# Performance work log

Measured on AMD Instinct MI355X. Metric: run time of the kernel, lower is better.

The kernel has to match this reference:

```python
import jax, jax.numpy as jnp
import numpy as np

# SAN Subtraction hyperparameters (from init_kwargs)
K = 7        # kernel_size
STRIDE = 1
PAD = 3
DIL = 1
PAD_MODE = 1  # 0 -> zero pad, 1 -> reflect pad


def setup_inputs() -> dict:
    key = jax.random.key(0)
    x = jax.random.normal(key, (4, 64, 112, 112), dtype=jnp.float32)
    return {"x": x}


def reference(x):
    """out[n,c,kk,p] = x_center[n,c,p] - neighbor_kk[n,c,p]  (SAN Subtraction).

    Returns (N, C, K*K, H_out*W_out).
    """
    N, C, H, W = x.shape
    H_out = (H + 2 * PAD - DIL * (K - 1) - 1) // STRIDE + 1
    W_out = (W + 2 * PAD - DIL * (K - 1) - 1) // STRIDE + 1

    mode = "reflect" if PAD_MODE == 1 else "constant"
    xp = jnp.pad(x, ((0, 0), (0, 0), (PAD, PAD), (PAD, PAD)), mode=mode)

    off = jnp.arange(K) * DIL                      # (K,)
    r = jnp.arange(H_out)[:, None] * STRIDE + off  # (H_out, K)
    c = jnp.arange(W_out)[:, None] * STRIDE + off  # (W_out, K)

    # gather neighbors: broadcast index -> (N, C, H_out, K, W_out, K)
    nb = xp[:, :, r[:, :, None, None], c[None, None, :, :]]
    # -> (N, C, K_row, K_col, H_out, W_out) -> (N, C, K*K, H_out*W_out)
    nb = nb.transpose(0, 1, 3, 5, 2, 4).reshape(N, C, K * K, H_out * W_out)

    # center: unfold with kernel 1, padding 0, given stride
    center = x[:, :, ::STRIDE, ::STRIDE][:, :, :H_out, :W_out]
    center = center.reshape(N, C, 1, H_out * W_out)

    return center - nb
```

## Files before the change

kernel.cpp:

```cpp
#include <hip/hip_runtime.h>


#define NC_   256
#define H_    112
#define W_    112
#define K_    7
#define PADV  3
#define HW    12544
#define W4_   28
#define K2_   49

typedef float vf4 __attribute__((ext_vector_type(4)));

__global__ __launch_bounds__(256) void san_sub_kernel(const float* __restrict__ x,
                                                      float* __restrict__ out) {
    int tid  = blockIdx.x * blockDim.x + threadIdx.x;
    int w4   = tid % W4_;
    int rest = tid / W4_;
    int h    = rest % H_;
    int nc   = rest / H_;

    int wbase = w4 * 4;
    const float* xc = x + nc * HW;

    vf4 center = *reinterpret_cast<const vf4*>(xc + h * W_ + wbase);

    float* outp = out + (size_t)nc * (K2_ * HW) + h * W_ + wbase;

    #pragma unroll
    for (int kh = 0; kh < K_; ++kh) {
        int r = h + kh - PADV;
        r = (r < 0) ? -r : r;
        r = (r > H_ - 1) ? (2 * (H_ - 1) - r) : r;
        const float* xrow = xc + r * W_;

        float win[10];
        #pragma unroll
        for (int t = 0; t < 10; ++t) {
            int col = wbase - PADV + t;
            col = (col < 0) ? -col : col;
            col = (col > W_ - 1) ? (2 * (W_ - 1) - col) : col;
            win[t] = xrow[col];
        }

        #pragma unroll
        for (int kw = 0; kw < K_; ++kw) {
            vf4 o;
            o.x = center.x - win[kw + 0];
            o.y = center.y - win[kw + 1];
            o.z = center.z - win[kw + 2];
            o.w = center.w - win[kw + 3];
            __builtin_nontemporal_store(
                o, reinterpret_cast<vf4*>(outp + (size_t)(kh * K_ + kw) * HW));
        }
    }
}

extern "C" void kernel_launch(void* const* d_in, const int* in_sizes, int n_in,
                              void* d_out, int out_size, void* d_ws, size_t ws_size,
                              hipStream_t stream) {
    const float* x = (const float*)d_in[0];
    float* out = (float*)d_out;
    dim3 grid(NC_ * H_ * W4_ / 256);
    dim3 block(256);
    san_sub_kernel<<<grid, block, 0, stream>>>(x, out);
}
```

Before: 619.8 us.

## Stage each channel plane in shared memory and split blocks by kernel row

```diff
diff --git a/kernel.cpp b/kernel.cpp
--- a/kernel.cpp
+++ b/kernel.cpp
@@ -7,51 +7,59 @@
 #define K_    7
 #define PADV  3
 #define HW    12544
-#define W4_   28
 #define K2_   49
 
 typedef float vf4 __attribute__((ext_vector_type(4)));
 
-__global__ __launch_bounds__(256) void san_sub_kernel(const float* __restrict__ x,
+__global__ __launch_bounds__(448) void san_sub_kernel(const float* __restrict__ x,
                                                       float* __restrict__ out) {
-    int tid  = blockIdx.x * blockDim.x + threadIdx.x;
-    int w4   = tid % W4_;
-    int rest = tid / W4_;
-    int h    = rest % H_;
-    int nc   = rest / H_;
+    __shared__ float sx[HW];
 
-    int wbase = w4 * 4;
-    const float* xc = x + nc * HW;
+    const int bid = blockIdx.x;
+    const int nc  = bid / K_;
+    const int kh  = bid % K_;
+    const int tid = threadIdx.x;
 
-    vf4 center = *reinterpret_cast<const vf4*>(xc + h * W_ + wbase);
-
-    float* outp = out + (size_t)nc * (K2_ * HW) + h * W_ + wbase;
+    const float* __restrict__ xc = x + (size_t)nc * HW;
 
     #pragma unroll
-    for (int kh = 0; kh < K_; ++kh) {
-        int r = h + kh - PADV;
-        r = (r < 0) ? -r : r;
-        r = (r > H_ - 1) ? (2 * (H_ - 1) - r) : r;
-        const float* xrow = xc + r * W_;
+    for (int s = 0; s < 7; ++s) {
+        int idx = s * 448 + tid;
+        vf4 v = *reinterpret_cast<const vf4*>(xc + idx * 4);
+        *reinterpret_cast<vf4*>(&sx[idx * 4]) = v;
+    }
+    __syncthreads();
 
-        float win[10];
-        #pragma unroll
-        for (int t = 0; t < 10; ++t) {
-            int col = wbase - PADV + t;
-            col = (col < 0) ? -col : col;
-            col = (col > W_ - 1) ? (2 * (W_ - 1) - col) : col;
-            win[t] = xrow[col];
+    const int trow = tid / 28;
+    const int w4   = tid % 28;
+    const int w    = w4 * 4;
+
+    for (int kw = 0; kw < K_; ++kw) {
+        int c0, c1, c2, c3;
+        {
+            int base = w + kw - PADV;
+            int cc;
+            cc = base + 0; cc = (cc < 0) ? -cc : cc; cc = (cc > W_-1) ? (2*(W_-1) - cc) : cc; c0 = cc;
+            cc = base + 1; cc = (cc < 0) ? -cc : cc; cc = (cc > W_-1) ? (2*(W_-1) - cc) : cc; c1 = cc;
+            cc = base + 2; cc = (cc < 0) ? -cc : cc; cc = (cc > W_-1) ? (2*(W_-1) - cc) : cc; c2 = cc;
+            cc = base + 3; cc = (cc < 0) ? -cc : cc; cc = (cc > W_-1) ? (2*(W_-1) - cc) : cc; c3 = cc;
         }
+        float* __restrict__ po = out + ((size_t)nc * K2_ + (size_t)(kh * K_ + kw)) * HW;
 
         #pragma unroll
-        for (int kw = 0; kw < K_; ++kw) {
+        for (int i = 0; i < 7; ++i) {
+            int h = i * 16 + trow;
+            int r = h + kh - PADV;
+            r = (r < 0) ? -r : r;
+            r = (r > H_-1) ? (2*(H_-1) - r) : r;
+            const float* srow = &sx[r * W_];
+            vf4 center = *reinterpret_cast<const vf4*>(&sx[h * W_ + w]);
             vf4 o;
-            o.x = center.x - win[kw + 0];
-            o.y = center.y - win[kw + 1];
-            o.z = center.z - win[kw + 2];
-            o.w = center.w - win[kw + 3];
-            __builtin_nontemporal_store(
-                o, reinterpret_cast<vf4*>(outp + (size_t)(kh * K_ + kw) * HW));
+            o.x = center.x - srow[c0];
+            o.y = center.y - srow[c1];
+            o.z = center.z - srow[c2];
+            o.w = center.w - srow[c3];
+            __builtin_nontemporal_store(o, reinterpret_cast<vf4*>(po + h * W_ + w));
         }
     }
 }
@@ -61,7 +69,7 @@
                               hipStream_t stream) {
     const float* x = (const float*)d_in[0];
     float* out = (float*)d_out;
-    dim3 grid(NC_ * H_ * W4_ / 256);
-    dim3 block(256);
+    dim3 grid(NC_ * K_);
+    dim3 block(448);
     san_sub_kernel<<<grid, block, 0, stream>>>(x, out);
 }
```

Result: no change. 620.6 us (+0.1%).
